# Kernel optimization log

Hardware: AMD Instinct MI355X
Metric: run time of the kernel (lower is better)

Reference implementation:

```python
import jax, jax.numpy as jnp
import numpy as np

E = 8       # n_experts
K = 2       # k_experts
D_IN = 1024
D_OUT = 1024
D_EXP = 2048
N = 16384   # tokens (batch*seq, forward requires 2D input)


def setup_inputs() -> dict:
    key = jax.random.key(0)
    ks = jax.random.split(key, 4)
    x = jax.random.normal(ks[0], (N, D_IN), jnp.float32)
    Wg = jax.random.normal(ks[1], (E, D_IN), jnp.float32) * 0.02      # router weight
    bg = jnp.zeros((E,), jnp.float32)                                  # router bias
    W_in = jax.random.normal(ks[2], (E, D_EXP, D_IN), jnp.float32) * 0.02
    b_in = jnp.zeros((E, D_EXP), jnp.float32)                          # w_in_bias_init=0.0
    W_out = jax.random.normal(ks[3], (E, D_OUT, D_EXP), jnp.float32) * 0.02  # bias=False
    return {"x": x, "Wg": Wg, "bg": bg, "W_in": W_in, "b_in": b_in, "W_out": W_out}


def moe_forward(x, Wg, bg, W_in, b_in, W_out):
    # Eval mode: gate jitter / solu jitter / dropouts are training-only no-ops.
    n = x.shape[0]
    # --- routing ---
    logits = x @ Wg.T + bg                                 # [N, E]
    probs = jax.nn.softmax(logits, axis=-1)
    mean_probs = probs.mean(axis=0)                        # [E]
    k_vals, k_idx = jax.lax.top_k(probs, K)                # [N, K]
    k_w = k_vals / k_vals.sum(axis=-1, keepdims=True)      # renormalized gate weights
    counts = jnp.bincount(k_idx.reshape(-1), length=E)     # [E] int
    load_balancing_loss = E * jnp.sum((counts.astype(x.dtype) / n) * mean_probs)
    # --- dispatch + expert w_in (loop over fixed small E; combine with one-hot mask) ---
    sel = jax.nn.one_hot(k_idx, E, dtype=x.dtype)          # [N, K, E]
    h = jnp.zeros((n, K, D_EXP), x.dtype)                  # preacts per (token, slot)
    for e in range(E):
        he = x @ W_in[e].T + b_in[e]                       # [N, D_EXP]
        h = h + sel[:, :, e][..., None] * he[:, None, :]
    # --- SoLU (eval): softmax(preacts) * preacts over hidden dim ---
    acts = jax.nn.softmax(h, axis=-1) * h                  # [N, K, D_EXP]
    # --- expert w_out (no bias) ---
    out = jnp.zeros((n, K, D_OUT), x.dtype)
    for e in range(E):
        oe = jnp.einsum('nkh,oh->nko', acts, W_out[e])
        out = out + sel[:, :, e][..., None] * oe
    # --- weighted combine over the K chosen experts ---
    outputs = (out * k_w[..., None]).sum(axis=1)           # [N, D_OUT]
    return outputs, load_balancing_loss


def reference(x, Wg, bg, W_in, b_in, W_out):
    return moe_forward(x, Wg, bg, W_in, b_in, W_out)
```

## Files before the change

### kernel.cpp

```cpp
#include <hip/hip_runtime.h>
#include <hip/hip_bf16.h>
#include <stdint.h>

#define E_EXP 8
#define NTOK  16384
#define DIN   1024
#define DEXP  2048
#define DOUT  1024
#define NSLOT (NTOK*2)
#define MAXT  264

#define AS_T  (128*64)
#define BS_T  (256*64)

typedef __attribute__((ext_vector_type(8))) short short8;
typedef __attribute__((ext_vector_type(8))) unsigned short ushort8;
typedef __attribute__((ext_vector_type(4))) unsigned short ushort4v;
typedef __attribute__((ext_vector_type(4))) float f32x4;

__device__ __forceinline__ unsigned short f2bf(float f){
  union { float f; uint32_t u; } v; v.f = f;
  uint32_t r = (v.u + 0x7FFFu + ((v.u >> 16) & 1u)) >> 16;
  return (unsigned short)r;
}
__device__ __forceinline__ float bf2f(unsigned short u){
  union { uint32_t u; float f; } v; v.u = ((uint32_t)u) << 16;
  return v.f;
}

__device__ __forceinline__ void async16(const void* g, void* l){
  __builtin_amdgcn_global_load_lds(
      (const __attribute__((address_space(1))) void*)g,
      (__attribute__((address_space(3))) void*)l, 16, 0, 0);
}

#define VMCNT6() asm volatile("s_waitcnt vmcnt(6)" ::: "memory")
#define VMCNT0() asm volatile("s_waitcnt vmcnt(0)" ::: "memory")
#define BARRIER() do { asm volatile("" ::: "memory"); __builtin_amdgcn_s_barrier(); asm volatile("" ::: "memory"); } while(0)

__global__ __launch_bounds__(256) void cast_bf16(const float* __restrict__ s,
                                                 unsigned short* __restrict__ d, int n){
  int i = (blockIdx.x*256 + threadIdx.x)*8;
  if (i >= n) return;
  float4 a = *(const float4*)(s+i);
  float4 b = *(const float4*)(s+i+4);
  ushort8 o;
  o[0]=f2bf(a.x); o[1]=f2bf(a.y); o[2]=f2bf(a.z); o[3]=f2bf(a.w);
  o[4]=f2bf(b.x); o[5]=f2bf(b.y); o[6]=f2bf(b.z); o[7]=f2bf(b.w);
  *(ushort8*)(d+i) = o;
}

__global__ __launch_bounds__(256) void router(
    const float* __restrict__ x, const float* __restrict__ Wg, const float* __restrict__ bg,
    unsigned short* __restrict__ xb,
    int* __restrict__ eidx, float* __restrict__ gw,
    int* __restrict__ counts, float* __restrict__ probsum)
{
  __shared__ float sWg[E_EXP*DIN];
  __shared__ float sps[E_EXP];
  __shared__ int   scnt[E_EXP];
  const int tid = threadIdx.x;
  for (int i = tid; i < E_EXP*DIN; i += 256) sWg[i] = Wg[i];
  if (tid < E_EXP){ sps[tid]=0.f; scnt[tid]=0; }
  __syncthreads();
  const int lane = tid & 63;
  const int wv   = tid >> 6;
  for (int it = 0; it < 16; ++it){
    const int token = blockIdx.x*64 + wv*16 + it;
    float4 xv[4];
#pragma unroll
    for (int j=0;j<4;++j) xv[j] = *(const float4*)&x[(size_t)token*DIN + j*256 + lane*4];
#pragma unroll
    for (int j=0;j<4;++j){
      ushort4v o;
      o[0]=f2bf(xv[j].x); o[1]=f2bf(xv[j].y); o[2]=f2bf(xv[j].z); o[3]=f2bf(xv[j].w);
      *(ushort4v*)&xb[(size_t)token*DIN + j*256 + lane*4] = o;
    }
    float p[E_EXP];
#pragma unroll
    for (int e2=0;e2<E_EXP;++e2){
      float s = 0.f;
#pragma unroll
      for (int j=0;j<4;++j){
        const float4 w4 = *(const float4*)&sWg[e2*DIN + j*256 + lane*4];
        s += xv[j].x*w4.x + xv[j].y*w4.y + xv[j].z*w4.z + xv[j].w*w4.w;
      }
      p[e2] = s;
    }
#pragma unroll
    for (int d=1; d<64; d<<=1){
#pragma unroll
      for (int e2=0;e2<E_EXP;++e2) p[e2] += __shfl_xor(p[e2], d);
    }
    if (lane == 0){
      float mx = -1e30f;
#pragma unroll
      for (int e2=0;e2<E_EXP;++e2){ p[e2] += bg[e2]; mx = fmaxf(mx, p[e2]); }
      float se = 0.f;
#pragma unroll
      for (int e2=0;e2<E_EXP;++e2){ p[e2] = __expf(p[e2]-mx); se += p[e2]; }
      const float inv = 1.f/se;
#pragma unroll
      for (int e2=0;e2<E_EXP;++e2){ p[e2] *= inv; atomicAdd(&sps[e2], p[e2]); }
      int i1 = 0;
#pragma unroll
      for (int e2=1;e2<E_EXP;++e2) if (p[e2] > p[i1]) i1 = e2;
      int i2 = (i1==0) ? 1 : 0;
#pragma unroll
      for (int e2=0;e2<E_EXP;++e2) if (e2 != i1 && p[e2] > p[i2]) i2 = e2;
      const float v1 = p[i1], v2 = p[i2], s12 = v1 + v2;
      eidx[2*token]   = i1; eidx[2*token+1] = i2;
      gw[2*token]     = v1/s12; gw[2*token+1] = v2/s12;
      atomicAdd(&scnt[i1], 1); atomicAdd(&scnt[i2], 1);
    }
  }
  __syncthreads();
  if (tid < E_EXP){ atomicAdd(&counts[tid], scnt[tid]); atomicAdd(&probsum[tid], sps[tid]); }
}

__global__ void finalize(const int* __restrict__ counts, const float* __restrict__ probsum,
                         float* __restrict__ loss_out, int* __restrict__ offs,
                         int* __restrict__ cursor, int* __restrict__ tile_e,
                         int* __restrict__ tile_row, int* __restrict__ ntiles)
{
  if (threadIdx.x != 0 || blockIdx.x != 0) return;
  int off = 0, nt = 0;
  float loss = 0.f;
  offs[0] = 0;
  for (int e2=0;e2<E_EXP;++e2){
    const int c = counts[e2];
    loss += (float)c * probsum[e2];
    cursor[e2] = 0;
    const int t = (c + 127) >> 7;
    for (int i=0;i<t;++i){ tile_e[nt] = e2; tile_row[nt] = off + i*128; ++nt; }
    off += c;
    offs[e2+1] = off;
  }
  *ntiles = nt;
  *loss_out = loss * (8.f/((float)NTOK*(float)NTOK));
}

__global__ __launch_bounds__(256) void scatter(const int* __restrict__ eidx,
    const int* __restrict__ offs, int* __restrict__ cursor,
    int* __restrict__ ptok, int* __restrict__ inv)
{
  const int t = blockIdx.x*256 + threadIdx.x;
  if (t >= NTOK) return;
#pragma unroll
  for (int s=0;s<2;++s){
    const int e2  = eidx[2*t+s];
    const int pos = offs[e2] + atomicAdd(&cursor[e2], 1);
    ptok[pos] = t;
    inv[2*t+s] = pos;
  }
}

__global__ __launch_bounds__(512, 2) void gemm1(
    const unsigned short* __restrict__ xb,
    const unsigned short* __restrict__ wib,
    const float* __restrict__ b_in,
    unsigned short* __restrict__ H,
    const int* __restrict__ ptok,
    const int* __restrict__ offs,
    const int* __restrict__ tile_e,
    const int* __restrict__ tile_row,
    const int* __restrict__ ntiles)
{
  if ((int)blockIdx.y >= *ntiles) return;
  const int e    = tile_e[blockIdx.y];
  const int row0 = tile_row[blockIdx.y];
  const int seg_end = offs[e+1];
  const int col0 = blockIdx.x * 256;

  __shared__ unsigned short As[3*AS_T];
  __shared__ unsigned short Bs[3*BS_T];

  const int tid  = threadIdx.x;
  const int lane = tid & 63;
  const int wv   = tid >> 6;
  const int wm   = wv >> 2;
  const int wn   = wv & 3;
  const int srow = tid >> 3;
  const int scol = ((tid & 7) ^ (srow & 7)) * 8;

  const unsigned short* ag[2];
#pragma unroll
  for (int i = 0; i < 2; ++i){
    int g = row0 + i*64 + srow; if (g > NSLOT-1) g = NSLOT-1;
    const int tok = ptok[g];
    ag[i] = xb + (size_t)tok*DIN + scol;
  }
  const unsigned short* bg4[4];
#pragma unroll
  for (int i = 0; i < 4; ++i)
    bg4[i] = wib + ((size_t)e*DEXP + col0 + i*64 + srow)*DIN + scol;
  float bias[4];
#pragma unroll
  for (int n = 0; n < 4; ++n)
    bias[n] = b_in[e*DEXP + col0 + wn*64 + n*16 + (lane&15)];

  f32x4 acc[4][4] = {};
  const int NK = DIN/64;

  const unsigned int aL0 = (wv*8)*64, aL1 = (64 + wv*8)*64;
  const unsigned int bL0 = (wv*8)*64, bL1 = (64+wv*8)*64, bL2 = (128+wv*8)*64, bL3 = (192+wv*8)*64;

#pragma unroll
  for (int t0 = 0; t0 < 2; ++t0){
    const int ko = t0*64;
    async16(ag[0]  + ko, &As[t0*AS_T + aL0]);
    async16(ag[1]  + ko, &As[t0*AS_T + aL1]);
    async16(bg4[0] + ko, &Bs[t0*BS_T + bL0]);
    async16(bg4[1] + ko, &Bs[t0*BS_T + bL1]);
    async16(bg4[2] + ko, &Bs[t0*BS_T + bL2]);
    async16(bg4[3] + ko, &Bs[t0*BS_T + bL3]);
  }
  VMCNT6();
  BARRIER();

  int cur = 0, stg = 2;
  for (int kt = 0; kt < NK; ++kt){
    const unsigned short* Ab = &As[cur*AS_T];
    const unsigned short* Bb = &Bs[cur*BS_T];
    const int doStage = (kt + 2 < NK);
    const int ko = (kt+2)*64;

    if (doStage){
      async16(ag[0]  + ko, &As[stg*AS_T + aL0]);
      async16(ag[1]  + ko, &As[stg*AS_T + aL1]);
      async16(bg4[0] + ko, &Bs[stg*BS_T + bL0]);
    }
    {
      const int ksl = (((lane>>4)) ^ (lane & 7)) * 8;
      short8 a[4], b[4];
#pragma unroll
      for (int m = 0; m < 4; ++m)
        a[m] = *(const short8*)&Ab[(wm*64 + m*16 + (lane&15))*64 + ksl];
#pragma unroll
      for (int n = 0; n < 4; ++n)
        b[n] = *(const short8*)&Bb[(wn*64 + n*16 + (lane&15))*64 + ksl];
      __builtin_amdgcn_s_setprio(1);
#pragma unroll
      for (int m = 0; m < 4; ++m)
#pragma unroll
        for (int n = 0; n < 4; ++n)
          acc[m][n] = __builtin_amdgcn_mfma_f32_16x16x32_bf16(a[m], b[n], acc[m][n], 0, 0, 0);
      __builtin_amdgcn_s_setprio(0);
    }

    if (doStage){
      async16(bg4[1] + ko, &Bs[stg*BS_T + bL1]);
      async16(bg4[2] + ko, &Bs[stg*BS_T + bL2]);
      async16(bg4[3] + ko, &Bs[stg*BS_T + bL3]);
    }
    {
      const int ksl = ((4 + (lane>>4)) ^ (lane & 7)) * 8;
      short8 a[4], b[4];
#pragma unroll
      for (int m = 0; m < 4; ++m)
        a[m] = *(const short8*)&Ab[(wm*64 + m*16 + (lane&15))*64 + ksl];
#pragma unroll
      for (int n = 0; n < 4; ++n)
        b[n] = *(const short8*)&Bb[(wn*64 + n*16 + (lane&15))*64 + ksl];
      __builtin_amdgcn_s_setprio(1);
#pragma unroll
      for (int m = 0; m < 4; ++m)
#pragma unroll
        for (int n = 0; n < 4; ++n)
          acc[m][n] = __builtin_amdgcn_mfma_f32_16x16x32_bf16(a[m], b[n], acc[m][n], 0, 0, 0);
      __builtin_amdgcn_s_setprio(0);
    }

    if (doStage) { VMCNT6(); } else { VMCNT0(); }
    BARRIER();
    cur = (cur == 2) ? 0 : cur + 1;
    stg = (stg == 2) ? 0 : stg + 1;
  }

#pragma unroll
  for (int m = 0; m < 4; ++m){
#pragma unroll
    for (int j = 0; j < 4; ++j){
      const int r = wm*64 + m*16 + (lane>>4)*4 + j;
      const int g = row0 + r;
      if (g < seg_end){
#pragma unroll
        for (int n = 0; n < 4; ++n){
          const int c = col0 + wn*64 + n*16 + (lane&15);
          H[(size_t)g*DEXP + c] = f2bf(acc[m][n][j] + bias[n]);
        }
      }
    }
  }
}

__global__ __launch_bounds__(256) void solu(unsigned short* __restrict__ H){
  const size_t row = blockIdx.x;
  unsigned short* hp = H + row*DEXP;
  const int tid  = threadIdx.x;
  const int lane = tid & 63;
  const int wv   = tid >> 6;
  const short8 hv = *(const short8*)&hp[tid*8];
  float f[8];
#pragma unroll
  for (int j=0;j<8;++j) f[j] = bf2f((unsigned short)hv[j]);
  float mx = f[0];
#pragma unroll
  for (int j=1;j<8;++j) mx = fmaxf(mx, f[j]);
  for (int d=1; d<64; d<<=1) mx = fmaxf(mx, __shfl_xor(mx, d));
  __shared__ float redm[4];
  __shared__ float reds[4];
  if (lane==0) redm[wv] = mx;
  __syncthreads();
  mx = fmaxf(fmaxf(redm[0],redm[1]), fmaxf(redm[2],redm[3]));
  float se = 0.f; float ex[8];
#pragma unroll
  for (int j=0;j<8;++j){ ex[j] = __expf(f[j]-mx); se += ex[j]; }
  for (int d=1; d<64; d<<=1) se += __shfl_xor(se, d);
  if (lane==0) reds[wv] = se;
  __syncthreads();
  se = reds[0]+reds[1]+reds[2]+reds[3];
  const float inv = 1.0f/se;
  ushort8 o;
#pragma unroll
  for (int j=0;j<8;++j) o[j] = f2bf(f[j]*ex[j]*inv);
  *(ushort8*)&hp[tid*8] = o;
}

__global__ __launch_bounds__(512, 2) void gemm2(
    const unsigned short* __restrict__ ACT,
    const unsigned short* __restrict__ wob,
    unsigned short* __restrict__ Oslot,
    const int* __restrict__ offs,
    const int* __restrict__ tile_e,
    const int* __restrict__ tile_row,
    const int* __restrict__ ntiles)
{
  if ((int)blockIdx.y >= *ntiles) return;
  const int e    = tile_e[blockIdx.y];
  const int row0 = tile_row[blockIdx.y];
  const int seg_end = offs[e+1];
  const int col0 = blockIdx.x * 256;

  __shared__ unsigned short As[3*AS_T];
  __shared__ unsigned short Bs[3*BS_T];

  const int tid  = threadIdx.x;
  const int lane = tid & 63;
  const int wv   = tid >> 6;
  const int wm   = wv >> 2;
  const int wn   = wv & 3;
  const int srow = tid >> 3;
  const int scol = ((tid & 7) ^ (srow & 7)) * 8;

  const unsigned short* ag[2];
#pragma unroll
  for (int i = 0; i < 2; ++i){
    int g = row0 + i*64 + srow; if (g > NSLOT-1) g = NSLOT-1;
    ag[i] = ACT + (size_t)g*DEXP + scol;
  }
  const unsigned short* bg4[4];
#pragma unroll
  for (int i = 0; i < 4; ++i)
    bg4[i] = wob + ((size_t)e*DOUT + col0 + i*64 + srow)*DEXP + scol;

  f32x4 acc[4][4] = {};
  const int NK = DEXP/64;

  const unsigned int aL0 = (wv*8)*64, aL1 = (64 + wv*8)*64;
  const unsigned int bL0 = (wv*8)*64, bL1 = (64+wv*8)*64, bL2 = (128+wv*8)*64, bL3 = (192+wv*8)*64;

#pragma unroll
  for (int t0 = 0; t0 < 2; ++t0){
    const int ko = t0*64;
    async16(ag[0]  + ko, &As[t0*AS_T + aL0]);
    async16(ag[1]  + ko, &As[t0*AS_T + aL1]);
    async16(bg4[0] + ko, &Bs[t0*BS_T + bL0]);
    async16(bg4[1] + ko, &Bs[t0*BS_T + bL1]);
    async16(bg4[2] + ko, &Bs[t0*BS_T + bL2]);
    async16(bg4[3] + ko, &Bs[t0*BS_T + bL3]);
  }
  VMCNT6();
  BARRIER();

  int cur = 0, stg = 2;
  for (int kt = 0; kt < NK; ++kt){
    const unsigned short* Ab = &As[cur*AS_T];
    const unsigned short* Bb = &Bs[cur*BS_T];
    const int doStage = (kt + 2 < NK);
    const int ko = (kt+2)*64;

    if (doStage){
      async16(ag[0]  + ko, &As[stg*AS_T + aL0]);
      async16(ag[1]  + ko, &As[stg*AS_T + aL1]);
      async16(bg4[0] + ko, &Bs[stg*BS_T + bL0]);
    }
    {
      const int ksl = (((lane>>4)) ^ (lane & 7)) * 8;
      short8 a[4], b[4];
#pragma unroll
      for (int m = 0; m < 4; ++m)
        a[m] = *(const short8*)&Ab[(wm*64 + m*16 + (lane&15))*64 + ksl];
#pragma unroll
      for (int n = 0; n < 4; ++n)
        b[n] = *(const short8*)&Bb[(wn*64 + n*16 + (lane&15))*64 + ksl];
      __builtin_amdgcn_s_setprio(1);
#pragma unroll
      for (int m = 0; m < 4; ++m)
#pragma unroll
        for (int n = 0; n < 4; ++n)
          acc[m][n] = __builtin_amdgcn_mfma_f32_16x16x32_bf16(a[m], b[n], acc[m][n], 0, 0, 0);
      __builtin_amdgcn_s_setprio(0);
    }

    if (doStage){
      async16(bg4[1] + ko, &Bs[stg*BS_T + bL1]);
      async16(bg4[2] + ko, &Bs[stg*BS_T + bL2]);
      async16(bg4[3] + ko, &Bs[stg*BS_T + bL3]);
    }
    {
      const int ksl = ((4 + (lane>>4)) ^ (lane & 7)) * 8;
      short8 a[4], b[4];
#pragma unroll
      for (int m = 0; m < 4; ++m)
        a[m] = *(const short8*)&Ab[(wm*64 + m*16 + (lane&15))*64 + ksl];
#pragma unroll
      for (int n = 0; n < 4; ++n)
        b[n] = *(const short8*)&Bb[(wn*64 + n*16 + (lane&15))*64 + ksl];
      __builtin_amdgcn_s_setprio(1);
#pragma unroll
      for (int m = 0; m < 4; ++m)
#pragma unroll
        for (int n = 0; n < 4; ++n)
          acc[m][n] = __builtin_amdgcn_mfma_f32_16x16x32_bf16(a[m], b[n], acc[m][n], 0, 0, 0);
      __builtin_amdgcn_s_setprio(0);
    }

    if (doStage) { VMCNT6(); } else { VMCNT0(); }
    BARRIER();
    cur = (cur == 2) ? 0 : cur + 1;
    stg = (stg == 2) ? 0 : stg + 1;
  }

#pragma unroll
  for (int m = 0; m < 4; ++m){
#pragma unroll
    for (int j = 0; j < 4; ++j){
      const int r = wm*64 + m*16 + (lane>>4)*4 + j;
      const int g = row0 + r;
      if (g < seg_end){
#pragma unroll
        for (int n = 0; n < 4; ++n){
          const int c = col0 + wn*64 + n*16 + (lane&15);
          Oslot[(size_t)g*DOUT + c] = f2bf(acc[m][n][j]);
        }
      }
    }
  }
}

__global__ __launch_bounds__(256) void combine(const unsigned short* __restrict__ Oslot,
    const int* __restrict__ inv, const float* __restrict__ gw, float* __restrict__ out)
{
  const int t    = blockIdx.x*4 + (threadIdx.x >> 6);
  const int lane = threadIdx.x & 63;
  const int p0 = inv[2*t], p1 = inv[2*t+1];
  const float w0 = gw[2*t], w1 = gw[2*t+1];
  const unsigned short* r0 = Oslot + (size_t)p0*DOUT + lane*16;
  const unsigned short* r1 = Oslot + (size_t)p1*DOUT + lane*16;
  ushort8 a0 = *(const ushort8*)r0;
  ushort8 a1 = *(const ushort8*)(r0 + 8);
  ushort8 b0 = *(const ushort8*)r1;
  ushort8 b1 = *(const ushort8*)(r1 + 8);
  float* op = out + (size_t)t*DOUT + lane*16;
  float4 o;
#pragma unroll
  for (int q = 0; q < 2; ++q){
    const ushort8 ua = q ? a1 : a0;
    const ushort8 ub = q ? b1 : b0;
#pragma unroll
    for (int h = 0; h < 2; ++h){
      o.x = w0*bf2f(ua[h*4+0]) + w1*bf2f(ub[h*4+0]);
      o.y = w0*bf2f(ua[h*4+1]) + w1*bf2f(ub[h*4+1]);
      o.z = w0*bf2f(ua[h*4+2]) + w1*bf2f(ub[h*4+2]);
      o.w = w0*bf2f(ua[h*4+3]) + w1*bf2f(ub[h*4+3]);
      *(float4*)(op + q*8 + h*4) = o;
    }
  }
}

extern "C" void kernel_launch(void* const* d_in, const int* in_sizes, int n_in,
                              void* d_out, int out_size, void* d_ws, size_t ws_size,
                              hipStream_t stream)
{
  const float* x     = (const float*)d_in[0];
  const float* Wg    = (const float*)d_in[1];
  const float* bgp   = (const float*)d_in[2];
  const float* W_in  = (const float*)d_in[3];
  const float* b_in  = (const float*)d_in[4];
  const float* W_out = (const float*)d_in[5];
  float* out = (float*)d_out;

  char* base = (char*)d_ws;
  size_t o = 0;
  unsigned short* xb  = (unsigned short*)(base + o); o += (size_t)NTOK*DIN*2;
  unsigned short* wib = (unsigned short*)(base + o); o += (size_t)E_EXP*DEXP*DIN*2;
  unsigned short* wob = (unsigned short*)(base + o); o += (size_t)E_EXP*DOUT*DEXP*2;
  unsigned short* H   = (unsigned short*)(base + o); o += (size_t)NSLOT*DEXP*2;
  unsigned short* Oslot = (unsigned short*)d_ws;
  int*   eidx    = (int*)(base + o);   o += (size_t)NSLOT*4;
  float* gw      = (float*)(base + o); o += (size_t)NSLOT*4;
  int*   ptok    = (int*)(base + o);   o += (size_t)NSLOT*4;
  int*   inv     = (int*)(base + o);   o += (size_t)NSLOT*4;
  int*   counts  = (int*)(base + o);   o += 32;
  float* probsum = (float*)(base + o); o += 32;
  int*   cursor  = (int*)(base + o);   o += 32;
  int*   offs    = (int*)(base + o);   o += 64;
  int*   tile_e  = (int*)(base + o);   o += (size_t)MAXT*4;
  int*   tile_row= (int*)(base + o);   o += (size_t)MAXT*4;
  int*   ntiles  = (int*)(base + o);   o += 64;

  hipMemsetAsync(counts, 0, 96, stream);

  cast_bf16<<<dim3(8192), 256, 0, stream>>>(W_in,  wib, E_EXP*DEXP*DIN);
  cast_bf16<<<dim3(8192), 256, 0, stream>>>(W_out, wob, E_EXP*DOUT*DEXP);

  router<<<dim3(256), 256, 0, stream>>>(x, Wg, bgp, xb, eidx, gw, counts, probsum);
  finalize<<<dim3(1), 64, 0, stream>>>(counts, probsum, out + (size_t)NTOK*DOUT,
                                       offs, cursor, tile_e, tile_row, ntiles);
  scatter<<<dim3(64), 256, 0, stream>>>(eidx, offs, cursor, ptok, inv);

  gemm1<<<dim3(DEXP/256, MAXT), 512, 0, stream>>>(xb, wib, b_in, H, ptok, offs,
                                                  tile_e, tile_row, ntiles);
  solu<<<dim3(NSLOT), 256, 0, stream>>>(H);
  gemm2<<<dim3(DOUT/256, MAXT), 512, 0, stream>>>(H, wob, Oslot, offs,
                                                  tile_e, tile_row, ntiles);
  combine<<<dim3(NTOK/4), 256, 0, stream>>>(Oslot, inv, gw, out);
}
```

Baseline: 908.3 us.

## Restructure GEMM K-loop barriers, merge weight casts, parallelize finalize

Both GEMM main loops are reorganised so each iteration starts with a barrier, issues all six async loads for stage kt+2, waits with vmcnt(12) or its tail equivalent, barriers again, then runs both k-halves of MFMA under one raised priority. This replaces the old interleaving of loads with compute. The two weight-cast launches are merged into one kernel, and the single-thread finalize loop becomes a 64-lane parallel tile-table build. The GEMM change adds a second barrier per iteration and no longer hides the issue of loads inside the compute. The other two changes only trim launch and serial overhead.

```diff
diff --git a/kernel.cpp b/kernel.cpp
--- a/kernel.cpp
+++ b/kernel.cpp
@@ -34,20 +34,26 @@
       (__attribute__((address_space(3))) void*)l, 16, 0, 0);
 }
 
-#define VMCNT6() asm volatile("s_waitcnt vmcnt(6)" ::: "memory")
-#define VMCNT0() asm volatile("s_waitcnt vmcnt(0)" ::: "memory")
+#define VMCNT12() asm volatile("s_waitcnt vmcnt(12)" ::: "memory")
+#define VMCNT6()  asm volatile("s_waitcnt vmcnt(6)"  ::: "memory")
+#define VMCNT0()  asm volatile("s_waitcnt vmcnt(0)"  ::: "memory")
 #define BARRIER() do { asm volatile("" ::: "memory"); __builtin_amdgcn_s_barrier(); asm volatile("" ::: "memory"); } while(0)
 
-__global__ __launch_bounds__(256) void cast_bf16(const float* __restrict__ s,
-                                                 unsigned short* __restrict__ d, int n){
+__global__ __launch_bounds__(256) void cast2(const float* __restrict__ a,
+                                             const float* __restrict__ b,
+                                             unsigned short* __restrict__ da,
+                                             unsigned short* __restrict__ db,
+                                             int na, int nb){
   int i = (blockIdx.x*256 + threadIdx.x)*8;
-  if (i >= n) return;
-  float4 a = *(const float4*)(s+i);
-  float4 b = *(const float4*)(s+i+4);
+  const float* s; unsigned short* d;
+  if (i < na){ s = a + i; d = da + i; }
+  else { int j = i - na; if (j >= nb) return; s = b + j; d = db + j; }
+  float4 x = *(const float4*)(s);
+  float4 y = *(const float4*)(s+4);
   ushort8 o;
-  o[0]=f2bf(a.x); o[1]=f2bf(a.y); o[2]=f2bf(a.z); o[3]=f2bf(a.w);
-  o[4]=f2bf(b.x); o[5]=f2bf(b.y); o[6]=f2bf(b.z); o[7]=f2bf(b.w);
-  *(ushort8*)(d+i) = o;
+  o[0]=f2bf(x.x); o[1]=f2bf(x.y); o[2]=f2bf(x.z); o[3]=f2bf(x.w);
+  o[4]=f2bf(y.x); o[5]=f2bf(y.y); o[6]=f2bf(y.z); o[7]=f2bf(y.w);
+  *(ushort8*)d = o;
 }
 
 __global__ __launch_bounds__(256) void router(
@@ -123,21 +129,31 @@
                          int* __restrict__ cursor, int* __restrict__ tile_e,
                          int* __restrict__ tile_row, int* __restrict__ ntiles)
 {
-  if (threadIdx.x != 0 || blockIdx.x != 0) return;
-  int off = 0, nt = 0;
-  float loss = 0.f;
-  offs[0] = 0;
-  for (int e2=0;e2<E_EXP;++e2){
-    const int c = counts[e2];
-    loss += (float)c * probsum[e2];
-    cursor[e2] = 0;
-    const int t = (c + 127) >> 7;
-    for (int i=0;i<t;++i){ tile_e[nt] = e2; tile_row[nt] = off + i*128; ++nt; }
-    off += c;
-    offs[e2+1] = off;
-  }
-  *ntiles = nt;
-  *loss_out = loss * (8.f/((float)NTOK*(float)NTOK));
+  const int lane = threadIdx.x;
+  int c[E_EXP];
+#pragma unroll
+  for (int e=0;e<E_EXP;++e) c[e] = counts[e];
+  int off[E_EXP+1], tb[E_EXP+1];
+  off[0]=0; tb[0]=0;
+#pragma unroll
+  for (int e=0;e<E_EXP;++e){ off[e+1]=off[e]+c[e]; tb[e+1]=tb[e]+((c[e]+127)>>7); }
+  if (lane==0){
+    float loss=0.f;
+#pragma unroll
+    for (int e=0;e<E_EXP;++e) loss += (float)c[e]*probsum[e];
+    *loss_out = loss * (8.f/((float)NTOK*(float)NTOK));
+    *ntiles = tb[E_EXP];
+    offs[E_EXP] = off[E_EXP];
+  }
+  if (lane < E_EXP){ cursor[lane]=0; offs[lane]=off[lane]; }
+  const int nt = tb[E_EXP];
+  for (int i=lane; i<nt; i+=64){
+    int e=0;
+#pragma unroll
+    for (int k=0;k<E_EXP-1;++k) if (i >= tb[k+1]) e = k+1;
+    tile_e[i]   = e;
+    tile_row[i] = off[e] + (i - tb[e])*128;
+  }
 }
 
 __global__ __launch_bounds__(256) void scatter(const int* __restrict__ eidx,
@@ -215,46 +231,32 @@
     async16(bg4[2] + ko, &Bs[t0*BS_T + bL2]);
     async16(bg4[3] + ko, &Bs[t0*BS_T + bL3]);
   }
-  VMCNT6();
-  BARRIER();
 
   int cur = 0, stg = 2;
   for (int kt = 0; kt < NK; ++kt){
-    const unsigned short* Ab = &As[cur*AS_T];
-    const unsigned short* Bb = &Bs[cur*BS_T];
-    const int doStage = (kt + 2 < NK);
-    const int ko = (kt+2)*64;
-
-    if (doStage){
+    BARRIER();
+    if (kt + 2 < NK){
+      const int ko = (kt+2)*64;
       async16(ag[0]  + ko, &As[stg*AS_T + aL0]);
       async16(ag[1]  + ko, &As[stg*AS_T + aL1]);
       async16(bg4[0] + ko, &Bs[stg*BS_T + bL0]);
-    }
-    {
-      const int ksl = (((lane>>4)) ^ (lane & 7)) * 8;
-      short8 a[4], b[4];
-#pragma unroll
-      for (int m = 0; m < 4; ++m)
-        a[m] = *(const short8*)&Ab[(wm*64 + m*16 + (lane&15))*64 + ksl];
-#pragma unroll
-      for (int n = 0; n < 4; ++n)
-        b[n] = *(const short8*)&Bb[(wn*64 + n*16 + (lane&15))*64 + ksl];
-      __builtin_amdgcn_s_setprio(1);
-#pragma unroll
-      for (int m = 0; m < 4; ++m)
-#pragma unroll
-        for (int n = 0; n < 4; ++n)
-          acc[m][n] = __builtin_amdgcn_mfma_f32_16x16x32_bf16(a[m], b[n], acc[m][n], 0, 0, 0);
-      __builtin_amdgcn_s_setprio(0);
-    }
-
-    if (doStage){
       async16(bg4[1] + ko, &Bs[stg*BS_T + bL1]);
       async16(bg4[2] + ko, &Bs[stg*BS_T + bL2]);
       async16(bg4[3] + ko, &Bs[stg*BS_T + bL3]);
-    }
-    {
-      const int ksl = ((4 + (lane>>4)) ^ (lane & 7)) * 8;
+      VMCNT12();
+    } else if (kt + 1 < NK){
+      VMCNT6();
+    } else {
+      VMCNT0();
+    }
+    BARRIER();
+
+    const unsigned short* Ab = &As[cur*AS_T];
+    const unsigned short* Bb = &Bs[cur*BS_T];
+    __builtin_amdgcn_s_setprio(1);
+#pragma unroll
+    for (int kk = 0; kk < 2; ++kk){
+      const int ksl = ((kk*4 + (lane>>4)) ^ (lane & 7)) * 8;
       short8 a[4], b[4];
 #pragma unroll
       for (int m = 0; m < 4; ++m)
@@ -262,17 +264,13 @@
 #pragma unroll
       for (int n = 0; n < 4; ++n)
         b[n] = *(const short8*)&Bb[(wn*64 + n*16 + (lane&15))*64 + ksl];
-      __builtin_amdgcn_s_setprio(1);
 #pragma unroll
       for (int m = 0; m < 4; ++m)
 #pragma unroll
         for (int n = 0; n < 4; ++n)
           acc[m][n] = __builtin_amdgcn_mfma_f32_16x16x32_bf16(a[m], b[n], acc[m][n], 0, 0, 0);
-      __builtin_amdgcn_s_setprio(0);
-    }
-
-    if (doStage) { VMCNT6(); } else { VMCNT0(); }
-    BARRIER();
+    }
+    __builtin_amdgcn_s_setprio(0);
     cur = (cur == 2) ? 0 : cur + 1;
     stg = (stg == 2) ? 0 : stg + 1;
   }
@@ -380,46 +378,32 @@
     async16(bg4[2] + ko, &Bs[t0*BS_T + bL2]);
     async16(bg4[3] + ko, &Bs[t0*BS_T + bL3]);
   }
-  VMCNT6();
-  BARRIER();
 
   int cur = 0, stg = 2;
   for (int kt = 0; kt < NK; ++kt){
-    const unsigned short* Ab = &As[cur*AS_T];
-    const unsigned short* Bb = &Bs[cur*BS_T];
-    const int doStage = (kt + 2 < NK);
-    const int ko = (kt+2)*64;
-
-    if (doStage){
+    BARRIER();
+    if (kt + 2 < NK){
+      const int ko = (kt+2)*64;
       async16(ag[0]  + ko, &As[stg*AS_T + aL0]);
       async16(ag[1]  + ko, &As[stg*AS_T + aL1]);
       async16(bg4[0] + ko, &Bs[stg*BS_T + bL0]);
-    }
-    {
-      const int ksl = (((lane>>4)) ^ (lane & 7)) * 8;
-      short8 a[4], b[4];
-#pragma unroll
-      for (int m = 0; m < 4; ++m)
-        a[m] = *(const short8*)&Ab[(wm*64 + m*16 + (lane&15))*64 + ksl];
-#pragma unroll
-      for (int n = 0; n < 4; ++n)
-        b[n] = *(const short8*)&Bb[(wn*64 + n*16 + (lane&15))*64 + ksl];
-      __builtin_amdgcn_s_setprio(1);
-#pragma unroll
-      for (int m = 0; m < 4; ++m)
-#pragma unroll
-        for (int n = 0; n < 4; ++n)
-          acc[m][n] = __builtin_amdgcn_mfma_f32_16x16x32_bf16(a[m], b[n], acc[m][n], 0, 0, 0);
-      __builtin_amdgcn_s_setprio(0);
-    }
-
-    if (doStage){
       async16(bg4[1] + ko, &Bs[stg*BS_T + bL1]);
       async16(bg4[2] + ko, &Bs[stg*BS_T + bL2]);
       async16(bg4[3] + ko, &Bs[stg*BS_T + bL3]);
-    }
-    {
-      const int ksl = ((4 + (lane>>4)) ^ (lane & 7)) * 8;
+      VMCNT12();
+    } else if (kt + 1 < NK){
+      VMCNT6();
+    } else {
+      VMCNT0();
+    }
+    BARRIER();
+
+    const unsigned short* Ab = &As[cur*AS_T];
+    const unsigned short* Bb = &Bs[cur*BS_T];
+    __builtin_amdgcn_s_setprio(1);
+#pragma unroll
+    for (int kk = 0; kk < 2; ++kk){
+      const int ksl = ((kk*4 + (lane>>4)) ^ (lane & 7)) * 8;
       short8 a[4], b[4];
 #pragma unroll
       for (int m = 0; m < 4; ++m)
@@ -427,17 +411,13 @@
 #pragma unroll
       for (int n = 0; n < 4; ++n)
         b[n] = *(const short8*)&Bb[(wn*64 + n*16 + (lane&15))*64 + ksl];
-      __builtin_amdgcn_s_setprio(1);
 #pragma unroll
       for (int m = 0; m < 4; ++m)
 #pragma unroll
         for (int n = 0; n < 4; ++n)
           acc[m][n] = __builtin_amdgcn_mfma_f32_16x16x32_bf16(a[m], b[n], acc[m][n], 0, 0, 0);
-      __builtin_amdgcn_s_setprio(0);
-    }
-
-    if (doStage) { VMCNT6(); } else { VMCNT0(); }
-    BARRIER();
+    }
+    __builtin_amdgcn_s_setprio(0);
     cur = (cur == 2) ? 0 : cur + 1;
     stg = (stg == 2) ? 0 : stg + 1;
   }
@@ -522,8 +502,8 @@
 
   hipMemsetAsync(counts, 0, 96, stream);
 
-  cast_bf16<<<dim3(8192), 256, 0, stream>>>(W_in,  wib, E_EXP*DEXP*DIN);
-  cast_bf16<<<dim3(8192), 256, 0, stream>>>(W_out, wob, E_EXP*DOUT*DEXP);
+  cast2<<<dim3(16384), 256, 0, stream>>>(W_in, W_out, wib, wob,
+                                         E_EXP*DEXP*DIN, E_EXP*DOUT*DEXP);
 
   router<<<dim3(256), 256, 0, stream>>>(x, Wg, bgp, xb, eidx, gw, counts, probsum);
   finalize<<<dim3(1), 64, 0, stream>>>(counts, probsum, out + (size_t)NTOK*DOUT,
```

Result: faster. 857.3 us (-5.6%).
